# Kernel tuning notes

Measured on AMD Instinct MI355X. Metric: run time of the kernel, lower is better.

The kernel has to match this reference:

```python
import jax, jax.numpy as jnp
import numpy as np

B, T, E, H = 32, 577, 1024, 16
D = E // H  # head_dim = 64

def setup_inputs() -> dict:
    key = jax.random.key(0)
    ks = jax.random.split(key, 5)
    s = 1.0 / np.sqrt(E)
    return {
        "x": jax.random.normal(ks[0], (B, T, E), dtype=jnp.float32),
        "Wq": jax.random.normal(ks[1], (E, E), dtype=jnp.float32) * s,
        "bq": jnp.zeros((E,), dtype=jnp.float32),
        "Wk": jax.random.normal(ks[2], (E, E), dtype=jnp.float32) * s,
        "bk": jnp.zeros((E,), dtype=jnp.float32),
        "Wv": jax.random.normal(ks[3], (E, E), dtype=jnp.float32) * s,
        "bv": jnp.zeros((E,), dtype=jnp.float32),
        "Wo": jax.random.normal(ks[4], (E, E), dtype=jnp.float32) * s,
        "bo": jnp.zeros((E,), dtype=jnp.float32),
    }

def reference(x, Wq, bq, Wk, bk, Wv, bv, Wo, bo):
    # Linear projections (torch Linear: x @ W.T + b; here W stored as [in,out])
    q = (x @ Wq + bq).reshape(B, T, H, D).transpose(0, 2, 1, 3)  # [B,H,T,D]
    k = (x @ Wk + bk).reshape(B, T, H, D).transpose(0, 2, 1, 3)
    v = (x @ Wv + bv).reshape(B, T, H, D).transpose(0, 2, 1, 3)
    scores = jnp.einsum('bhqd,bhkd->bhqk', q, k) / jnp.sqrt(jnp.float32(D))
    att = jax.nn.softmax(scores, axis=-1)  # dropout is identity in eval
    out = jnp.einsum('bhqk,bhkd->bhqd', att, v)
    out = out.transpose(0, 2, 1, 3).reshape(B, T, E)
    return out @ Wo + bo
```

## Files before the change

kernel.cpp:

```cpp
#include <hip/hip_runtime.h>
#include <cmath>

#define BDIM 32
#define TDIM 577
#define TPAD 640
#define EDIM 1024
#define HDIM 16
#define DDIM 64
#define MDIM (BDIM * TDIM)
#define MTILES 145
#define MPAD (MTILES * 128)

typedef unsigned short u16;
typedef __bf16 bf16x8 __attribute__((ext_vector_type(8)));
typedef float f32x4 __attribute__((ext_vector_type(4)));
typedef u16 u16x8 __attribute__((ext_vector_type(8)));

__device__ __forceinline__ u16 f2bf(float f) {
    unsigned int u = __float_as_uint(f);
    u = (u + 0x7FFFu + ((u >> 16) & 1u)) >> 16;
    return (u16)u;
}

__device__ __forceinline__ void gload_lds16(const void* g, void* l) {
    __builtin_amdgcn_global_load_lds(
        (const __attribute__((address_space(1))) unsigned int*)g,
        (__attribute__((address_space(3))) unsigned int*)l, 16, 0, 0);
}

__global__ __launch_bounds__(256) void cast_x(const float* __restrict__ x,
                                              u16* __restrict__ o, int nelem)
{
    int i = (blockIdx.x * 256 + threadIdx.x) * 8;
    if (i >= nelem) return;
    float4 a = *(const float4*)(x + i);
    float4 b = *(const float4*)(x + i + 4);
    u16x8 r;
    r[0] = f2bf(a.x); r[1] = f2bf(a.y); r[2] = f2bf(a.z); r[3] = f2bf(a.w);
    r[4] = f2bf(b.x); r[5] = f2bf(b.y); r[6] = f2bf(b.z); r[7] = f2bf(b.w);
    *(u16x8*)(o + i) = r;
}

__global__ __launch_bounds__(256) void cast_wt(
    const float* __restrict__ W0, const float* __restrict__ W1,
    const float* __restrict__ W2, const float* __restrict__ W3,
    u16* __restrict__ T0, u16* __restrict__ T1,
    u16* __restrict__ T2, u16* __restrict__ T3)
{
    __shared__ float tile[32][33];
    const int z = blockIdx.z;
    const float* __restrict__ W = (z == 0) ? W0 : (z == 1) ? W1 : (z == 2) ? W2 : W3;
    u16* __restrict__ T = (z == 0) ? T0 : (z == 1) ? T1 : (z == 2) ? T2 : T3;
    const int bn = blockIdx.x * 32;
    const int bk = blockIdx.y * 32;
    const int tx = threadIdx.x & 31, ty = threadIdx.x >> 5;
#pragma unroll
    for (int p = 0; p < 4; ++p) {
        int k = bk + p * 8 + ty;
        tile[p * 8 + ty][tx] = W[(size_t)k * EDIM + bn + tx];
    }
    __syncthreads();
#pragma unroll
    for (int p = 0; p < 4; ++p) {
        int n = bn + p * 8 + ty;
        T[(size_t)n * EDIM + bk + tx] = f2bf(tile[tx][p * 8 + ty]);
    }
}

__global__ __launch_bounds__(256, 4) void gemm_bf16(
    const u16* __restrict__ A,
    const u16* __restrict__ W0, const u16* __restrict__ W1, const u16* __restrict__ W2,
    const float* __restrict__ b0, const float* __restrict__ b1, const float* __restrict__ b2,
    void* __restrict__ o0, void* __restrict__ o1, void* __restrict__ o2,
    int mode)
{
    __shared__ u16 As[128 * 64];
    __shared__ u16 Bs[128 * 64];

    const int z = blockIdx.z;
    const u16* __restrict__ Wt     = (z == 0) ? W0 : ((z == 1) ? W1 : W2);
    const float* __restrict__ bias = (z == 0) ? b0 : ((z == 1) ? b1 : b2);
    void* __restrict__ dst         = (z == 0) ? o0 : ((z == 1) ? o1 : o2);

    const int tid = threadIdx.x;
    const int wave = tid >> 6;
    const int lane = tid & 63;
    const int mlane = lane & 15;
    const int quad = lane >> 4;
    const int wm = wave >> 1;
    const int wn = wave & 1;
    const int m0 = blockIdx.y * 128;
    const int n0 = blockIdx.x * 128;

    f32x4 acc[4][4];
#pragma unroll
    for (int i = 0; i < 4; ++i)
#pragma unroll
        for (int j = 0; j < 4; ++j) acc[i][j] = (f32x4)(0.f);

    for (int k0 = 0; k0 < EDIM; k0 += 64) {
#pragma unroll
        for (int r = 0; r < 4; ++r) {
            int c = r * 256 + tid;
            int p = c >> 9, row = (c >> 2) & 127, j4 = c & 3;
            int koff = k0 + p * 32 + j4 * 8;
            gload_lds16(A + (size_t)(m0 + row) * EDIM + koff,
                        &As[(r * 256 + wave * 64) * 8]);
            gload_lds16(Wt + (size_t)(n0 + row) * EDIM + koff,
                        &Bs[(r * 256 + wave * 64) * 8]);
        }
        __syncthreads();

#pragma unroll
        for (int ks = 0; ks < 2; ++ks) {
            bf16x8 af[4], bfr[4];
#pragma unroll
            for (int t = 0; t < 4; ++t) {
                af[t]  = *(const bf16x8*)&As[ks * 4096 + (wm * 64 + t * 16 + mlane) * 32 + quad * 8];
                bfr[t] = *(const bf16x8*)&Bs[ks * 4096 + (wn * 64 + t * 16 + mlane) * 32 + quad * 8];
            }
#pragma unroll
            for (int i = 0; i < 4; ++i)
#pragma unroll
                for (int j = 0; j < 4; ++j)
                    acc[i][j] = __builtin_amdgcn_mfma_f32_16x16x32_bf16(af[i], bfr[j], acc[i][j], 0, 0, 0);
        }
        __syncthreads();
    }

#pragma unroll
    for (int j = 0; j < 4; ++j) {
        int n = n0 + wn * 64 + j * 16 + mlane;
        float bv = bias[n];
        if (mode == 1) {
            float* df = (float*)dst;
#pragma unroll
            for (int i = 0; i < 4; ++i) {
                int mb = m0 + wm * 64 + i * 16 + quad * 4;
#pragma unroll
                for (int r = 0; r < 4; ++r) {
                    int gm = mb + r;
                    if (gm < MDIM) df[(size_t)gm * EDIM + n] = acc[i][j][r] + bv;
                }
            }
        } else {
            u16* db = (u16*)dst;
            int h = n >> 6, d = n & 63;
#pragma unroll
            for (int i = 0; i < 4; ++i) {
                int mb = m0 + wm * 64 + i * 16 + quad * 4;
#pragma unroll
                for (int r = 0; r < 4; ++r) {
                    int gm = mb + r;
                    if (gm < MDIM) {
                        int b = gm / TDIM, t = gm - b * TDIM;
                        u16 val = f2bf(acc[i][j][r] + bv);
                        if (z == 2)
                            db[((size_t)(b * HDIM + h) * DDIM + d) * TPAD + t] = val;
                        else
                            db[((size_t)(b * HDIM + h) * TPAD + t) * DDIM + d] = val;
                    }
                }
            }
        }
    }
}

__global__ __launch_bounds__(256) void attn_mfma(
    const u16* __restrict__ qg, const u16* __restrict__ kg,
    const u16* __restrict__ vtg, u16* __restrict__ outg)
{
    __shared__ u16 Qs[4096];
    __shared__ u16 Ks[4096];
    __shared__ u16 Vts[4096];
    __shared__ u16 Ps[4608];

    const int tid = threadIdx.x;
    const int wave = tid >> 6;
    const int lane = tid & 63;
    const int ml = lane & 15;
    const int quad = lane >> 4;
    const int h = blockIdx.y, b = blockIdx.z;
    const int q0 = blockIdx.x * 64;
    const u16* qb = qg + ((size_t)b * HDIM + h) * TPAD * DDIM;
    const u16* kb = kg + ((size_t)b * HDIM + h) * TPAD * DDIM;
    const u16* vb = vtg + ((size_t)b * HDIM + h) * DDIM * TPAD;

#pragma unroll
    for (int r = 0; r < 2; ++r) {
        int c = r * 256 + tid;
        int row = (c >> 2) & 63, kc = c >> 8, d8 = c & 3;
        gload_lds16(qb + (size_t)(q0 + row) * DDIM + kc * 32 + d8 * 8,
                    &Qs[(r * 256 + wave * 64) * 8]);
    }
    __syncthreads();

    bf16x8 aq0 = *(const bf16x8*)&Qs[(wave * 16 + ml) * 32 + quad * 8];
    bf16x8 aq1 = *(const bf16x8*)&Qs[2048 + (wave * 16 + ml) * 32 + quad * 8];

    f32x4 oacc[4];
#pragma unroll
    for (int dt = 0; dt < 4; ++dt) oacc[dt] = (f32x4)(0.f);
    float m_i[4], l_i[4];
#pragma unroll
    for (int r = 0; r < 4; ++r) { m_i[r] = -INFINITY; l_i[r] = 0.f; }

    for (int kv0 = 0; kv0 < TDIM; kv0 += 64) {
        __syncthreads();
#pragma unroll
        for (int r = 0; r < 2; ++r) {
            int c = r * 256 + tid;
            int row = (c >> 2) & 63, kc = c >> 8, d8 = c & 3;
            gload_lds16(kb + (size_t)(kv0 + row) * DDIM + kc * 32 + d8 * 8,
                        &Ks[(r * 256 + wave * 64) * 8]);
            gload_lds16(vb + (size_t)row * TPAD + kv0 + kc * 32 + d8 * 8,
                        &Vts[(r * 256 + wave * 64) * 8]);
        }
        __syncthreads();

        f32x4 sacc[4];
#pragma unroll
        for (int jt = 0; jt < 4; ++jt) {
            bf16x8 bk0 = *(const bf16x8*)&Ks[(jt * 16 + ml) * 32 + quad * 8];
            bf16x8 bk1 = *(const bf16x8*)&Ks[2048 + (jt * 16 + ml) * 32 + quad * 8];
            f32x4 sa = (f32x4)(0.f);
            sa = __builtin_amdgcn_mfma_f32_16x16x32_bf16(aq0, bk0, sa, 0, 0, 0);
            sa = __builtin_amdgcn_mfma_f32_16x16x32_bf16(aq1, bk1, sa, 0, 0, 0);
            sacc[jt] = sa;
        }

        float p[4][4];
#pragma unroll
        for (int r = 0; r < 4; ++r) {
            float cm = -INFINITY;
#pragma unroll
            for (int jt = 0; jt < 4; ++jt) {
                bool valid = (kv0 + jt * 16 + ml) < TDIM;
                float sv = valid ? sacc[jt][r] * 0.125f : -INFINITY;
                p[jt][r] = sv;
                cm = fmaxf(cm, sv);
            }
            cm = fmaxf(cm, __shfl_xor(cm, 1, 64));
            cm = fmaxf(cm, __shfl_xor(cm, 2, 64));
            cm = fmaxf(cm, __shfl_xor(cm, 4, 64));
            cm = fmaxf(cm, __shfl_xor(cm, 8, 64));
            float mn = fmaxf(m_i[r], cm);
            float alpha = __expf(m_i[r] - mn);
            float rs = 0.f;
#pragma unroll
            for (int jt = 0; jt < 4; ++jt) {
                float e = __expf(p[jt][r] - mn);
                p[jt][r] = e;
                rs += e;
            }
            rs += __shfl_xor(rs, 1, 64);
            rs += __shfl_xor(rs, 2, 64);
            rs += __shfl_xor(rs, 4, 64);
            rs += __shfl_xor(rs, 8, 64);
            l_i[r] = l_i[r] * alpha + rs;
            m_i[r] = mn;
#pragma unroll
            for (int dt = 0; dt < 4; ++dt) oacc[dt][r] *= alpha;
        }

#pragma unroll
        for (int jt = 0; jt < 4; ++jt)
#pragma unroll
            for (int r = 0; r < 4; ++r)
                Ps[wave * 1152 + (jt >> 1) * 576 + (quad * 4 + r) * 36 + (jt & 1) * 16 + ml]
                    = f2bf(p[jt][r]);
        __syncthreads();

        bf16x8 pf0 = *(const bf16x8*)&Ps[wave * 1152 + ml * 36 + quad * 8];
        bf16x8 pf1 = *(const bf16x8*)&Ps[wave * 1152 + 576 + ml * 36 + quad * 8];

#pragma unroll
        for (int dt = 0; dt < 4; ++dt) {
            bf16x8 bv0 = *(const bf16x8*)&Vts[(dt * 16 + ml) * 32 + quad * 8];
            bf16x8 bv1 = *(const bf16x8*)&Vts[2048 + (dt * 16 + ml) * 32 + quad * 8];
            oacc[dt] = __builtin_amdgcn_mfma_f32_16x16x32_bf16(pf0, bv0, oacc[dt], 0, 0, 0);
            oacc[dt] = __builtin_amdgcn_mfma_f32_16x16x32_bf16(pf1, bv1, oacc[dt], 0, 0, 0);
        }
    }

#pragma unroll
    for (int r = 0; r < 4; ++r) {
        int t = q0 + wave * 16 + quad * 4 + r;
        if (t >= TDIM) continue;
        float inv = 1.f / l_i[r];
        size_t rowoff = ((size_t)b * TDIM + t) * EDIM + h * DDIM;
#pragma unroll
        for (int dt = 0; dt < 4; ++dt)
            outg[rowoff + dt * 16 + ml] = f2bf(oacc[dt][r] * inv);
    }
}

extern "C" void kernel_launch(void* const* d_in, const int* in_sizes, int n_in,
                              void* d_out, int out_size, void* d_ws, size_t ws_size,
                              hipStream_t stream)
{
    const float* x  = (const float*)d_in[0];
    const float* Wq = (const float*)d_in[1];
    const float* bq = (const float*)d_in[2];
    const float* Wk = (const float*)d_in[3];
    const float* bk = (const float*)d_in[4];
    const float* Wv = (const float*)d_in[5];
    const float* bv = (const float*)d_in[6];
    const float* Wo = (const float*)d_in[7];
    const float* bo = (const float*)d_in[8];
    float* out = (float*)d_out;

    const size_t hsz = (size_t)BDIM * HDIM * TPAD * DDIM;
    u16* qb  = (u16*)d_ws;
    u16* kb  = qb + hsz;
    u16* vtb = kb + hsz;
    u16* xb  = vtb + hsz;
    u16* abb = xb;
    u16* wtq = xb + (size_t)MPAD * EDIM;
    u16* wtk = wtq + (size_t)EDIM * EDIM;
    u16* wtv = wtk + (size_t)EDIM * EDIM;
    u16* wto = wtv + (size_t)EDIM * EDIM;

    cast_x<<<(MDIM * EDIM / 8 + 255) / 256, 256, 0, stream>>>(x, xb, MDIM * EDIM);
    cast_wt<<<dim3(32, 32, 4), 256, 0, stream>>>(Wq, Wk, Wv, Wo, wtq, wtk, wtv, wto);

    gemm_bf16<<<dim3(EDIM / 128, MTILES, 3), 256, 0, stream>>>(
        xb, wtq, wtk, wtv, bq, bk, bv, (void*)qb, (void*)kb, (void*)vtb, 0);

    attn_mfma<<<dim3(TPAD / 64, HDIM, BDIM), 256, 0, stream>>>(qb, kb, vtb, abb);

    gemm_bf16<<<dim3(EDIM / 128, MTILES, 1), 256, 0, stream>>>(
        abb, wto, wto, wto, bo, bo, bo, (void*)out, (void*)out, (void*)out, 1);
}
```

Baseline: 610.6 us.

## Replace 128x128 GEMM with pipelined 256x256 tile, 512-thread kernel

Replaces the projection GEMM with a 256x256-tile, 8-wave kernel. It double-buffers LDS with direct global-to-LDS loads issued inside four compute phases, using explicit vmcnt/lgkmcnt waits, sched barriers and setprio around the MFMA bursts. It also remaps block indices so contiguous work chunks are grouped by blockIdx modulo 8, which looks aimed at the chip's XCD layout. The larger tile raises data reuse and overlaps loads with compute, at the cost of more registers, two blocks per CU, and reads past the padded A rows into the next workspace buffer.

```diff
diff --git a/kernel.cpp b/kernel.cpp
--- a/kernel.cpp
+++ b/kernel.cpp
@@ -10,6 +10,8 @@
 #define MDIM (BDIM * TDIM)
 #define MTILES 145
 #define MPAD (MTILES * 128)
+#define MT256 73
+#define NTILES_K 16
 
 typedef unsigned short u16;
 typedef __bf16 bf16x8 __attribute__((ext_vector_type(8)));
@@ -27,6 +29,10 @@
         (const __attribute__((address_space(1))) unsigned int*)g,
         (__attribute__((address_space(3))) unsigned int*)l, 16, 0, 0);
 }
+
+#define SB()  __builtin_amdgcn_sched_barrier(0)
+#define BAR() __builtin_amdgcn_s_barrier()
+#define WAIT_LGKM0() asm volatile("s_waitcnt lgkmcnt(0)" ::: "memory")
 
 __global__ __launch_bounds__(256) void cast_x(const float* __restrict__ x,
                                               u16* __restrict__ o, int nelem)
@@ -67,66 +73,117 @@
     }
 }
 
-__global__ __launch_bounds__(256, 4) void gemm_bf16(
+__global__ __launch_bounds__(512, 2) void gemm256(
     const u16* __restrict__ A,
     const u16* __restrict__ W0, const u16* __restrict__ W1, const u16* __restrict__ W2,
     const float* __restrict__ b0, const float* __restrict__ b1, const float* __restrict__ b2,
     void* __restrict__ o0, void* __restrict__ o1, void* __restrict__ o2,
     int mode)
 {
-    __shared__ u16 As[128 * 64];
-    __shared__ u16 Bs[128 * 64];
+    __shared__ u16 lds[2][2][2][8192];
 
     const int z = blockIdx.z;
     const u16* __restrict__ Wt     = (z == 0) ? W0 : ((z == 1) ? W1 : W2);
     const float* __restrict__ bias = (z == 0) ? b0 : ((z == 1) ? b1 : b2);
     void* __restrict__ dst         = (z == 0) ? o0 : ((z == 1) ? o1 : o2);
 
-    const int tid = threadIdx.x;
-    const int wave = tid >> 6;
-    const int lane = tid & 63;
+    const int tid   = threadIdx.x;
+    const int wave  = tid >> 6;
+    const int lane  = tid & 63;
     const int mlane = lane & 15;
-    const int quad = lane >> 4;
-    const int wm = wave >> 1;
-    const int wn = wave & 1;
-    const int m0 = blockIdx.y * 128;
-    const int n0 = blockIdx.x * 128;
-
-    f32x4 acc[4][4];
-#pragma unroll
-    for (int i = 0; i < 4; ++i)
+    const int quad  = lane >> 4;
+    const int wm = wave >> 2;
+    const int wn = wave & 3;
+
+    const int loc = blockIdx.y * gridDim.x + blockIdx.x;
+    const int cc = loc & 7, cp = loc >> 3;
+    const int work = (cc < 4 ? cc * 37 : 148 + (cc - 4) * 36) + cp;
+    const int n0 = (work & 3) * 256;
+    const int m0 = (work >> 2) * 256;
+
+    f32x4 acc[8][4];
+#pragma unroll
+    for (int i = 0; i < 8; ++i)
 #pragma unroll
         for (int j = 0; j < 4; ++j) acc[i][j] = (f32x4)(0.f);
 
-    for (int k0 = 0; k0 < EDIM; k0 += 64) {
-#pragma unroll
-        for (int r = 0; r < 4; ++r) {
-            int c = r * 256 + tid;
-            int p = c >> 9, row = (c >> 2) & 127, j4 = c & 3;
-            int koff = k0 + p * 32 + j4 * 8;
-            gload_lds16(A + (size_t)(m0 + row) * EDIM + koff,
-                        &As[(r * 256 + wave * 64) * 8]);
-            gload_lds16(Wt + (size_t)(n0 + row) * EDIM + koff,
-                        &Bs[(r * 256 + wave * 64) * 8]);
-        }
-        __syncthreads();
-
-#pragma unroll
-        for (int ks = 0; ks < 2; ++ks) {
-            bf16x8 af[4], bfr[4];
-#pragma unroll
-            for (int t = 0; t < 4; ++t) {
-                af[t]  = *(const bf16x8*)&As[ks * 4096 + (wm * 64 + t * 16 + mlane) * 32 + quad * 8];
-                bfr[t] = *(const bf16x8*)&Bs[ks * 4096 + (wn * 64 + t * 16 + mlane) * 32 + quad * 8];
-            }
-#pragma unroll
-            for (int i = 0; i < 4; ++i)
-#pragma unroll
-                for (int j = 0; j < 4; ++j)
-                    acc[i][j] = __builtin_amdgcn_mfma_f32_16x16x32_bf16(af[i], bfr[j], acc[i][j], 0, 0, 0);
-        }
-        __syncthreads();
-    }
+    auto stage = [&](int db, int mat, int hf, int t) {
+        if (t >= NTILES_K) return;
+        const u16* src = (mat == 0) ? (A  + (size_t)(m0 + hf * 128) * EDIM)
+                                    : (Wt + (size_t)(n0 + hf * 128) * EDIM);
+        const int kb = t * 64;
+#pragma unroll
+        for (int r = 0; r < 2; ++r) {
+            int c = r * 512 + tid;
+            int ks = c >> 9, row = (c >> 2) & 127, j4 = c & 3;
+            gload_lds16(src + (size_t)row * EDIM + kb + ks * 32 + j4 * 8,
+                        &lds[db][mat][hf][(r * 512 + wave * 64) * 8]);
+        }
+    };
+
+    const int arow = wm * 64 + mlane;
+    const int brow = (wn & 1) * 64 + mlane;
+    const int bhf  = wn >> 1;
+    bf16x8 bq[4][2];
+
+#define GPHASE(RB, QI, STAGE_STMT)                                             \
+    do {                                                                       \
+        const u16* la = &lds[cb][0][RB][0];                                    \
+        bf16x8 af[2][2];                                                       \
+        _Pragma("unroll") for (int ri2 = 0; ri2 < 2; ++ri2)                    \
+            _Pragma("unroll") for (int ks = 0; ks < 2; ++ks)                   \
+                af[ri2][ks] = *(const bf16x8*)&la[ks * 4096 +                  \
+                    (arow + ((QI) * 2 + ri2) * 16) * 32 + quad * 8];           \
+        STAGE_STMT;                                                            \
+        SB(); BAR(); WAIT_LGKM0(); SB();                                       \
+        __builtin_amdgcn_s_setprio(1);                                         \
+        _Pragma("unroll") for (int ri2 = 0; ri2 < 2; ++ri2)                    \
+            _Pragma("unroll") for (int j = 0; j < 4; ++j)                      \
+                _Pragma("unroll") for (int ks = 0; ks < 2; ++ks)               \
+                    acc[(RB) * 4 + (QI) * 2 + ri2][j] =                        \
+                        __builtin_amdgcn_mfma_f32_16x16x32_bf16(               \
+                            af[ri2][ks], bq[j][ks],                            \
+                            acc[(RB) * 4 + (QI) * 2 + ri2][j], 0, 0, 0);       \
+        __builtin_amdgcn_s_setprio(0);                                         \
+    } while (0)
+
+    stage(0, 0, 0, 0);
+    stage(0, 1, 0, 0);
+    stage(0, 1, 1, 0);
+    stage(0, 0, 1, 0);
+    stage(1, 1, 0, 1);
+    stage(1, 1, 1, 1);
+    stage(1, 0, 0, 1);
+    asm volatile("s_waitcnt vmcnt(6)" ::: "memory");
+    SB(); BAR();
+
+    for (int t = 0; t < NTILES_K; ++t) {
+        const int cb = t & 1;
+        const int nb = cb ^ 1;
+
+        {
+            const u16* lb = &lds[cb][1][bhf][0];
+#pragma unroll
+            for (int j = 0; j < 4; ++j)
+#pragma unroll
+                for (int ks = 0; ks < 2; ++ks)
+                    bq[j][ks] = *(const bf16x8*)&lb[ks * 4096 +
+                        (brow + j * 16) * 32 + quad * 8];
+        }
+        GPHASE(0, 0, stage(nb, 0, 1, t + 1));
+        SB(); BAR();
+        GPHASE(0, 1, stage(cb, 1, 0, t + 2));
+        SB(); BAR();
+        GPHASE(1, 0, stage(cb, 1, 1, t + 2));
+        SB(); BAR();
+        GPHASE(1, 1, stage(cb, 0, 0, t + 2));
+        if (t < NTILES_K - 1) {
+            if (t == NTILES_K - 2) { asm volatile("s_waitcnt vmcnt(0)" ::: "memory"); }
+            else                   { asm volatile("s_waitcnt vmcnt(6)" ::: "memory"); }
+            SB(); BAR();
+        }
+    }
+#undef GPHASE
 
 #pragma unroll
     for (int j = 0; j < 4; ++j) {
@@ -135,26 +192,26 @@
         if (mode == 1) {
             float* df = (float*)dst;
 #pragma unroll
-            for (int i = 0; i < 4; ++i) {
-                int mb = m0 + wm * 64 + i * 16 + quad * 4;
+            for (int mr = 0; mr < 8; ++mr) {
+                int mb = m0 + wm * 64 + (mr >> 2) * 128 + (mr & 3) * 16 + quad * 4;
 #pragma unroll
                 for (int r = 0; r < 4; ++r) {
                     int gm = mb + r;
-                    if (gm < MDIM) df[(size_t)gm * EDIM + n] = acc[i][j][r] + bv;
+                    if (gm < MDIM) df[(size_t)gm * EDIM + n] = acc[mr][j][r] + bv;
                 }
             }
         } else {
             u16* db = (u16*)dst;
             int h = n >> 6, d = n & 63;
 #pragma unroll
-            for (int i = 0; i < 4; ++i) {
-                int mb = m0 + wm * 64 + i * 16 + quad * 4;
+            for (int mr = 0; mr < 8; ++mr) {
+                int mb = m0 + wm * 64 + (mr >> 2) * 128 + (mr & 3) * 16 + quad * 4;
 #pragma unroll
                 for (int r = 0; r < 4; ++r) {
                     int gm = mb + r;
                     if (gm < MDIM) {
                         int b = gm / TDIM, t = gm - b * TDIM;
-                        u16 val = f2bf(acc[i][j][r] + bv);
+                        u16 val = f2bf(acc[mr][j][r] + bv);
                         if (z == 2)
                             db[((size_t)(b * HDIM + h) * DDIM + d) * TPAD + t] = val;
                         else
@@ -324,11 +381,11 @@
     cast_x<<<(MDIM * EDIM / 8 + 255) / 256, 256, 0, stream>>>(x, xb, MDIM * EDIM);
     cast_wt<<<dim3(32, 32, 4), 256, 0, stream>>>(Wq, Wk, Wv, Wo, wtq, wtk, wtv, wto);
 
-    gemm_bf16<<<dim3(EDIM / 128, MTILES, 3), 256, 0, stream>>>(
+    gemm256<<<dim3(EDIM / 256, MT256, 3), 512, 0, stream>>>(
         xb, wtq, wtk, wtv, bq, bk, bv, (void*)qb, (void*)kb, (void*)vtb, 0);
 
     attn_mfma<<<dim3(TPAD / 64, HDIM, BDIM), 256, 0, stream>>>(qb, kb, vtb, abb);
 
-    gemm_bf16<<<dim3(EDIM / 128, MTILES, 1), 256, 0, stream>>>(
+    gemm256<<<dim3(EDIM / 256, MT256, 1), 512, 0, stream>>>(
         abb, wto, wto, wto, bo, bo, bo, (void*)out, (void*)out, (void*)out, 1);
 }
```

After: 649.0 us. 1.06x slower.
